# Kernel tuning notes

Measured on AMD Instinct MI355X. Metric: run time of the kernel, lower is better.

Reference implementation:

```python
import jax, jax.numpy as jnp
import numpy as np

NEG = -9e15
EPS = 1e-5

# GraphAttention (classic GAT layer): h = xW; e_ij = LeakyReLU(a1.h_i + a2.h_j);
# attention = softmax(where(adj>0, e, -9e15)); out = attention @ h.
# The torch code builds one big block-diagonal adjacency; off-block entries get
# -9e15 and underflow to exactly 0 after softmax, so batched per-block GAT is
# numerically identical and avoids the O((B*N)^2) dense waste.

def gat(x, adj, W, a1, a2):
    h = jnp.einsum('bnf,fh->bnh', x, W)
    e = jax.nn.leaky_relu(jnp.einsum('bnh,h->bn', h, a1)[:, :, None]
                          + jnp.einsum('bnh,h->bn', h, a2)[:, None, :], 0.2)
    att = jax.nn.softmax(jnp.where(adj > 0, e, NEG), axis=-1)
    return jnp.einsum('bnm,bmh->bnh', att, h)

def mlp(x, W1, b1, W2, b2):
    return jax.nn.relu(x @ W1 + b1) @ W2 + b2


def setup_inputs() -> dict:
    key = jax.random.key(0)
    ks = iter(jax.random.split(key, 40))
    B, NV, NO = 8, 500, 1500
    DV, DO, H = 512, 32, 128

    def mat(din, dout):
        return jax.random.normal(next(ks), (din, dout), jnp.float32) / np.sqrt(din)

    def vec(d):
        return jax.random.normal(next(ks), (d,), jnp.float32) * 0.1

    inp = {
        'vis_memory': jax.random.normal(next(ks), (B, NV, DV), jnp.float32),
        'obj_memory': jax.random.normal(next(ks), (B, NO, DO), jnp.float32),
        'vis_adj': jax.random.uniform(next(ks), (B, NV, NV), jnp.float32),
        'obj_adj': jax.random.uniform(next(ks), (B, NO, NO), jnp.float32),
        'object_A_OV': jax.random.uniform(next(ks), (B, NO, NV), jnp.float32),
        # GAT layers
        'Wv1': mat(DV, H), 'av1a': vec(H), 'av1b': vec(H),
        'Wv2': mat(H, H),  'av2a': vec(H), 'av2b': vec(H),
        'Wo1': mat(DO, H), 'ao1a': vec(H), 'ao1b': vec(H),
        'Wo2': mat(H, H),  'ao2a': vec(H), 'ao2b': vec(H),
        # globalTobject / objectTglobal MLPs
        'g2o_W1': mat(H, H), 'g2o_b1': jnp.zeros((H,), jnp.float32),
        'g2o_W2': mat(H, H), 'g2o_b2': jnp.zeros((H,), jnp.float32),
        'o2g_W1': mat(H, H), 'o2g_b1': jnp.zeros((H,), jnp.float32),
        'o2g_W2': mat(H, H), 'o2g_b2': jnp.zeros((H,), jnp.float32),
        # output projections
        'img_W': mat(H, DV), 'img_b': jnp.zeros((DV,), jnp.float32),
        'obj_W': mat(H, DO), 'obj_b': jnp.zeros((DO,), jnp.float32),
    }
    return inp


def reference(vis_memory, obj_memory, vis_adj, obj_adj, object_A_OV,
              Wv1, av1a, av1b, Wv2, av2a, av2b,
              Wo1, ao1a, ao1b, Wo2, ao2a, ao2b,
              g2o_W1, g2o_b1, g2o_W2, g2o_b2,
              o2g_W1, o2g_b1, o2g_W2, o2g_b2,
              img_W, img_b, obj_W, obj_b):
    # cross adjacencies (block-diagonal in torch -> batched here)
    vo = jnp.swapaxes(object_A_OV, 1, 2)            # (B, NV, NO)
    vo = vo / (vo.sum(2, keepdims=True) + EPS)
    ov = jnp.swapaxes(vo, 1, 2)                     # (B, NO, NV)
    ov = ov / (ov.sum(2, keepdims=True) + EPS)

    v1 = jax.nn.relu(gat(vis_memory, vis_adj, Wv1, av1a, av1b))
    o1 = jax.nn.relu(gat(obj_memory, obj_adj, Wo1, ao1a, ao1b))
    vis = v1 + mlp(jnp.einsum('bvo,boh->bvh', vo, o1), o2g_W1, o2g_b1, o2g_W2, o2g_b2)
    obj = o1 + mlp(jnp.einsum('bov,bvh->boh', ov, v1), g2o_W1, g2o_b1, g2o_W2, g2o_b2)

    v2 = jax.nn.relu(gat(vis, vis_adj, Wv2, av2a, av2b))
    o2 = jax.nn.relu(gat(obj, obj_adj, Wo2, ao2a, ao2b))
    vis = v2 + mlp(jnp.einsum('bvo,boh->bvh', vo, o2), o2g_W1, o2g_b1, o2g_W2, o2g_b2)
    obj = o2 + mlp(jnp.einsum('bov,bvh->boh', ov, v2), g2o_W1, g2o_b1, g2o_W2, g2o_b2)

    vis_out = vis @ img_W + img_b                   # (B, NV, DV)
    obj_out = obj @ obj_W + obj_b                   # (B, NO, DO)
    return (vis_out, obj_out)
```

## Files before the change

### kernel.cpp

```cpp
#include <hip/hip_runtime.h>
#include <math.h>

#define EPSV 1e-5f
#define HD 128
#define IT 64
#define JT 32
#define WP 68
#define CCH 16
#define THR 256

typedef __attribute__((address_space(3))) uint32_t lds_u32_t;
typedef __attribute__((address_space(1))) uint32_t gbl_u32_t;
typedef __attribute__((ext_vector_type(8))) short bf16x8;
typedef __attribute__((ext_vector_type(4))) float f32x4;

__device__ __forceinline__ void async_copy16(const float* g, float* l) {
    __builtin_amdgcn_global_load_lds((const gbl_u32_t*)g, (lds_u32_t*)l, 16, 0, 0);
}

__device__ __forceinline__ void stage_tile_async(const float* gsrc, float* lds, int t) {
    int wv = t >> 6, lane = t & 63;
#pragma unroll
    for (int it = 0; it < 4; ++it) {
        int c = it * 4 + wv;
        async_copy16(gsrc + c * 256 + lane * 4, lds + c * 256);
    }
}

__device__ __forceinline__ void stage_8k(const void* g, void* l, int t) {
    const float* gf = (const float*)g; float* lf = (float*)l;
    async_copy16(gf + t * 4, lf + t * 4);
    async_copy16(gf + t * 4 + 1024, lf + t * 4 + 1024);
}

__device__ __forceinline__ unsigned int f2bf(float f) {
    return __builtin_bit_cast(unsigned int, f) >> 16;
}

__device__ __forceinline__ unsigned short rne_bf16(float f) {
    unsigned int u = __builtin_bit_cast(unsigned int, f);
    u += 0x7FFFu + ((u >> 16) & 1u);
    return (unsigned short)(u >> 16);
}

struct WprepP { const float *W, *a1, *a2; unsigned short* WT; float *wa1, *wa2; int K; };
struct XprepP { const float* X; unsigned short* Xbf; const float *wa1, *wa2;
                float *sa, *sb; int rows; };
struct GmfP   { const unsigned short *Xbf, *WT; unsigned short* hT; int N, tilesJ; };
struct AggP  { const unsigned int* mask; const float *sa, *sb, *sm; const unsigned short* hT;
               float* out; int N, tiles, tilesJ; };
struct CrossP{ const float *A, *src, *rs1; float *pp; int iN, jN, tiles, tps; };
struct MlpP  { const float *pp, *scale; int S; const float *W1, *b1, *W2, *b2, *res;
               float *out; int rows; };


__global__ void colsum_part_k(const float* __restrict__ A, float* __restrict__ s1p,
                              int B, int NO, int NV) {
    int v = blockIdx.x * 256 + threadIdx.x;
    int c = blockIdx.y, b = blockIdx.z;
    if (v >= NV) return;
    int chunk = (NO + CCH - 1) / CCH;
    int o0 = c * chunk;
    int o1 = o0 + chunk; if (o1 > NO) o1 = NO;
    const float* Ab = A + (size_t)b * NO * NV + v;
    float s = 0.f;
    for (int o = o0; o < o1; ++o) s += Ab[(size_t)o * NV];
    s1p[((size_t)b * CCH + c) * NV + v] = s;
}

__global__ void colsum_fin_k(const float* __restrict__ s1p, float* __restrict__ rs1,
                             int B, int NV) {
    int idx = blockIdx.x * 256 + threadIdx.x;
    if (idx >= B * NV) return;
    int b = idx / NV, v = idx - b * NV;
    float s = 0.f;
    for (int c = 0; c < CCH; ++c) s += s1p[((size_t)b * CCH + c) * NV + v];
    rs1[idx] = 1.f / (s + EPSV);
}

__global__ void rowsum_inv_k(const float* __restrict__ A, const float* __restrict__ rs1,
                             float* __restrict__ rs2, int B, int NO, int NV) {
    int row = blockIdx.x * (blockDim.x >> 6) + (threadIdx.x >> 6);
    int lane = threadIdx.x & 63;
    if (row >= B * NO) return;
    int b = row / NO;
    const float* Ar = A + (size_t)row * NV;
    const float* r1 = rs1 + (size_t)b * NV;
    float s = 0.f;
    for (int v = lane; v < NV; v += 64) s += Ar[v] * r1[v];
    for (int off = 32; off; off >>= 1) s += __shfl_xor(s, off, 64);
    if (lane == 0) rs2[row] = 1.f / (s + EPSV);
}

template<int N, int TILESJ>
__global__ __launch_bounds__(256)
void maskg_k(const float* __restrict__ adj, unsigned int* __restrict__ maskT) {
    int tid = blockIdx.x * 256 + threadIdx.x;
    int w = tid % TILESJ;
    int rowid = tid / TILESJ;
    if (rowid >= 8 * N) return;
    int b = rowid / N, i = rowid - b * N;
    int j0 = w * 32;
    const float* src = adj + (size_t)rowid * N + j0;
    unsigned int bits = 0u;
    if (j0 + 32 <= N) {
#pragma unroll
        for (int q = 0; q < 8; ++q) {
            float4 v = ((const float4*)src)[q];
            bits |= (v.x > 0.f ? 1u : 0u) << (q * 4 + 0);
            bits |= (v.y > 0.f ? 1u : 0u) << (q * 4 + 1);
            bits |= (v.z > 0.f ? 1u : 0u) << (q * 4 + 2);
            bits |= (v.w > 0.f ? 1u : 0u) << (q * 4 + 3);
        }
    } else {
#pragma unroll
        for (int r = 0; r < 32; ++r)
            if (j0 + r < N) bits |= (src[r] > 0.f ? 1u : 0u) << r;
    }
    maskT[((size_t)b * TILESJ + w) * N + i] = bits;
}

__global__ __launch_bounds__(256)
void wprep_k(WprepP p0, WprepP p1, WprepP p2, WprepP p3, int e0, int e1, int e2) {
    __shared__ float lw[32][129];
    __shared__ float a1s[128], a2s[128];
    int bid = blockIdx.x;
    const WprepP& P = bid < e0 ? p0 : bid < e1 ? p1 : bid < e2 ? p2 : p3;
    int lb = bid < e0 ? bid : bid < e1 ? bid - e0 : bid < e2 ? bid - e1 : bid - e2;
    int k0 = lb * 32, K = P.K;
    int t = threadIdx.x;
    if (t < 128) { a1s[t] = P.a1[t]; a2s[t] = P.a2[t]; }
    for (int idx = t; idx < 32 * 32; idx += 256) {
        int kk = idx >> 5, c4 = idx & 31;
        float4 v = ((const float4*)(P.W + (size_t)(k0 + kk) * 128))[c4];
        lw[kk][c4 * 4 + 0] = v.x; lw[kk][c4 * 4 + 1] = v.y;
        lw[kk][c4 * 4 + 2] = v.z; lw[kk][c4 * 4 + 3] = v.w;
    }
    __syncthreads();
    int kk = t >> 3, g = t & 7;
    float s1 = 0.f, s2 = 0.f;
    for (int c = g; c < 128; c += 8) {
        float w = lw[kk][c];
        s1 = fmaf(w, a1s[c], s1);
        s2 = fmaf(w, a2s[c], s2);
    }
    s1 += __shfl_xor(s1, 1, 64); s1 += __shfl_xor(s1, 2, 64); s1 += __shfl_xor(s1, 4, 64);
    s2 += __shfl_xor(s2, 1, 64); s2 += __shfl_xor(s2, 2, 64); s2 += __shfl_xor(s2, 4, 64);
    if (g == 0) { P.wa1[k0 + kk] = s1; P.wa2[k0 + kk] = s2; }
    for (int idx = t; idx < 4096; idx += 256) {
        int c = idx >> 5, k = idx & 31;
        P.WT[(size_t)c * K + k0 + k] = rne_bf16(lw[k][c]);
    }
}

template<int K>
__device__ void xprep_body(const XprepP& P, int lb) {
    int t = threadIdx.x, wv = t >> 6, lane = t & 63;
    int row = lb * 4 + wv;
    if (row >= P.rows) return;
    const float4* x4 = (const float4*)(P.X + (size_t)row * K);
    const float4* w14 = (const float4*)P.wa1;
    const float4* w24 = (const float4*)P.wa2;
    unsigned short* xb = P.Xbf + (size_t)row * K;
    float s1 = 0.f, s2 = 0.f;
    constexpr int K4 = K / 4;
    constexpr int NI = (K4 + 63) / 64;
#pragma unroll
    for (int i = 0; i < NI; ++i) {
        int k4 = i * 64 + lane;
        if ((K4 % 64 == 0) || (k4 < K4)) {
            float4 x = x4[k4];
            float4 a = w14[k4];
            float4 b = w24[k4];
            s1 += x.x * a.x + x.y * a.y + x.z * a.z + x.w * a.w;
            s2 += x.x * b.x + x.y * b.y + x.z * b.z + x.w * b.w;
            ushort4 p = make_ushort4(rne_bf16(x.x), rne_bf16(x.y),
                                     rne_bf16(x.z), rne_bf16(x.w));
            *(ushort4*)(xb + (size_t)k4 * 4) = p;
        }
    }
#pragma unroll
    for (int off = 32; off; off >>= 1) {
        s1 += __shfl_xor(s1, off, 64);
        s2 += __shfl_xor(s2, off, 64);
    }
    if (lane == 0) { P.sa[row] = s1; P.sb[row] = s2; }
}

template<int KV, int KO>
__global__ __launch_bounds__(256)
void xprep2_k(XprepP V, XprepP O, int GV) {
    int bid = blockIdx.x;
    if (bid < GV) xprep_body<KV>(V, bid);
    else          xprep_body<KO>(O, bid - GV);
}

template<int K>
__device__ void gmf_body(const GmfP& P, int lb) {
    int tilesJ = P.tilesJ, N = P.N;
    int b = lb / tilesJ, jt = lb - b * tilesJ;
    int t = threadIdx.x, wv = t >> 6, lane = t & 63;
    int ml = lane & 15, quad = lane >> 4;
    const unsigned short* xb = P.Xbf + ((size_t)b * N + (size_t)jt * 32) * K;
    const unsigned short* wt0 = P.WT + (size_t)(wv * 32 + ml) * K;
    const unsigned short* wt1 = wt0 + (size_t)16 * K;
    const unsigned short* xb0 = xb + (size_t)ml * K;
    const unsigned short* xb1 = xb + (size_t)(16 + ml) * K;
    f32x4 acc00 = {0.f, 0.f, 0.f, 0.f}, acc01 = acc00, acc10 = acc00, acc11 = acc00;
#pragma unroll 4
    for (int kt = 0; kt < K / 32; ++kt) {
        int kk = kt * 32 + quad * 8;
        bf16x8 a0 = *(const bf16x8*)(wt0 + kk);
        bf16x8 a1 = *(const bf16x8*)(wt1 + kk);
        bf16x8 b0 = *(const bf16x8*)(xb0 + kk);
        bf16x8 b1 = *(const bf16x8*)(xb1 + kk);
        acc00 = __builtin_amdgcn_mfma_f32_16x16x32_bf16(a0, b0, acc00, 0, 0, 0);
        acc01 = __builtin_amdgcn_mfma_f32_16x16x32_bf16(a0, b1, acc01, 0, 0, 0);
        acc10 = __builtin_amdgcn_mfma_f32_16x16x32_bf16(a1, b0, acc10, 0, 0, 0);
        acc11 = __builtin_amdgcn_mfma_f32_16x16x32_bf16(a1, b1, acc11, 0, 0, 0);
    }
    unsigned short* hb = P.hT + (size_t)(b * tilesJ + jt) * 4096;
    int nvalid = N - jt * 32; if (nvalid > 32) nvalid = 32;
    bool ok0 = ml < nvalid, ok1 = (16 + ml) < nvalid;
    int c0 = wv * 32 + quad * 4;
#pragma unroll
    for (int r = 0; r < 4; ++r) {
        int ca = c0 + r, cb = c0 + 16 + r;
        int swa = ((ca >> 1) & 3) << 3, swb = ((cb >> 1) & 3) << 3;
        hb[ca * 32 + (ml ^ swa)]        = ok0 ? rne_bf16(acc00[r]) : 0;
        hb[ca * 32 + ((16 + ml) ^ swa)] = ok1 ? rne_bf16(acc01[r]) : 0;
        hb[cb * 32 + (ml ^ swb)]        = ok0 ? rne_bf16(acc10[r]) : 0;
        hb[cb * 32 + ((16 + ml) ^ swb)] = ok1 ? rne_bf16(acc11[r]) : 0;
    }
}

template<int KV, int KO>
__global__ __launch_bounds__(256)
void gmf2_k(GmfP V, GmfP O, int GV) {
    int bid = blockIdx.x;
    if (bid < GV) gmf_body<KV>(V, bid);
    else          gmf_body<KO>(O, bid - GV);
}

__global__ __launch_bounds__(256)
void sbmax2_k(const float* __restrict__ sbV, float* __restrict__ smV,
              const float* __restrict__ sbO, float* __restrict__ smO,
              int NV, int NO) {
    __shared__ float red[256];
    int b0 = blockIdx.x, t = threadIdx.x;
    const float* sb; float* out; int N;
    if (b0 < 8) { sb = sbV + (size_t)b0 * NV; out = smV + b0; N = NV; }
    else        { sb = sbO + (size_t)(b0 - 8) * NO; out = smO + (b0 - 8); N = NO; }
    float m = -INFINITY;
    for (int j = t; j < N; j += 256) m = fmaxf(m, sb[j]);
    red[t] = m; __syncthreads();
    for (int s = 128; s; s >>= 1) {
        if (t < s) red[t] = fmaxf(red[t], red[t + s]);
        __syncthreads();
    }
    if (t == 0) *out = red[0];
}

struct SharedAggM {
    unsigned short hsT[3][128][32];
    unsigned short wsA[2][4][64][8];
    unsigned int mask_s[48][64];
    float sb_s[48 * 32];
    float sa_s[IT], m_s[IT], z_s[IT];
};

__device__ void agg_body(SharedAggM& sm, const AggP& P, int lbid) {
    int tiles = P.tiles;
    int b = lbid / tiles;
    int i0 = (lbid - b * tiles) * IT;
    int N = P.N;
    int T = P.tilesJ;
    int t = threadIdx.x;
    if (t < IT) {
        int i = i0 + t;
        float s = (i < N) ? P.sa[(size_t)b * N + i] : 0.f;
        sm.sa_s[t] = s;
        float e = s + P.sm[b];
        sm.m_s[t] = e > 0.f ? e : 0.2f * e;
    }
    for (int idx = t; idx < (T << 6); idx += 256) {
        int w = idx >> 6, r = idx & 63;
        int ir = i0 + r;
        sm.mask_s[w][r] = (ir < N)
            ? P.mask[((size_t)b * T + w) * N + ir] : 0u;
    }
    const float* sbb = P.sb + (size_t)b * N;
    for (int idx = t; idx < (T << 5); idx += 256) {
        sm.sb_s[idx] = (idx < N) ? sbb[idx] : 0.f;
    }
    __syncthreads();
    const unsigned short* hTb = P.hT + (size_t)b * T * 4096;
    stage_8k(hTb, &sm.hsT[0][0][0], t);
    stage_8k(hTb + 4096, &sm.hsT[1][0][0], t);

    int wv = t >> 6, lane = t & 63;
    int il = t >> 2, j4 = (t & 3) * 4;
    int q0 = j4 >> 3, i0w = j4 & 7, wrow = il & 15;
    int nquad = lane >> 4, nlow = lane & 15;
    int nq2 = (nquad ^ ((nlow >> 1) & 3)) * 8;
    f32x4 acc[8];
#pragma unroll
    for (int nt = 0; nt < 8; ++nt)
#pragma unroll
        for (int r = 0; r < 4; ++r) acc[nt][r] = 0.f;
    float zacc = 0.f;
    const float4* sb4 = (const float4*)sm.sb_s;
    for (int tt = 0; tt < T; ++tt) {
        int cur = tt - (tt / 3) * 3;
        unsigned int mw = sm.mask_s[tt][il];
        float4 sA = sb4[tt * 8 + (t & 3)];
        float4 sB = sb4[tt * 8 + (t & 3) + 4];
        float sai = sm.sa_s[il], m = sm.m_s[il];
#pragma unroll
        for (int k = 0; k < 2; ++k) {
            float sv[4];
            { float4 s4 = k ? sB : sA; sv[0] = s4.x; sv[1] = s4.y; sv[2] = s4.z; sv[3] = s4.w; }
            float w_[4];
#pragma unroll
            for (int r = 0; r < 4; ++r) {
                float e = sai + sv[r];
                e = e > 0.f ? e : 0.2f * e;
                float ww = __expf(e - m);
                ww = ((mw >> (j4 + k * 16 + r)) & 1u) ? ww : 0.f;
                zacc += ww;
                w_[r] = ww;
            }
            unsigned int lo = f2bf(w_[0]) | (__builtin_bit_cast(unsigned int, w_[1]) & 0xFFFF0000u);
            unsigned int hi = f2bf(w_[2]) | (__builtin_bit_cast(unsigned int, w_[3]) & 0xFFFF0000u);
            *(uint2*)&sm.wsA[tt & 1][wv][wrow + 16 * (q0 + 2 * k)][i0w] = make_uint2(lo, hi);
        }
        if (tt + 1 < T) asm volatile("s_waitcnt vmcnt(2) lgkmcnt(0)" ::: "memory");
        else            asm volatile("s_waitcnt vmcnt(0) lgkmcnt(0)" ::: "memory");
        __builtin_amdgcn_s_barrier();
        asm volatile("" ::: "memory");
        if (tt + 2 < T) {
            int nb = tt + 2; nb -= (nb / 3) * 3;
            stage_8k(hTb + (size_t)(tt + 2) * 4096, &sm.hsT[nb][0][0], t);
        }
        bf16x8 afrag = *(const bf16x8*)&sm.wsA[tt & 1][wv][lane][0];
#pragma unroll
        for (int nt = 0; nt < 8; ++nt) {
            bf16x8 bfrag = *(const bf16x8*)&sm.hsT[cur][nt * 16 + nlow][nq2];
            acc[nt] = __builtin_amdgcn_mfma_f32_16x16x32_bf16(afrag, bfrag, acc[nt], 0, 0, 0);
        }
    }
    zacc += __shfl_xor(zacc, 1, 64);
    zacc += __shfl_xor(zacc, 2, 64);
    if ((t & 3) == 0) sm.z_s[il] = zacc;
    __syncthreads();
    float inv[4];
#pragma unroll
    for (int r = 0; r < 4; ++r) inv[r] = 1.f / sm.z_s[wv * 16 + nquad * 4 + r];
    float* outb = P.out + (size_t)b * N * HD;
#pragma unroll
    for (int nt = 0; nt < 8; ++nt)
#pragma unroll
        for (int r = 0; r < 4; ++r) {
            int row = i0 + wv * 16 + nquad * 4 + r;
            if (row < N)
                outb[(size_t)row * HD + nt * 16 + nlow] = fmaxf(acc[nt][r] * inv[r], 0.f);
        }
}

__global__ __launch_bounds__(256)
void agg2_k(AggP V, AggP O, int GVb) {
    __shared__ SharedAggM sm;
    int bid = blockIdx.x;
    if (bid < GVb) agg_body(sm, V, bid);
    else           agg_body(sm, O, bid - GVb);
}

__device__ __forceinline__ void tile_fma256(const float (*hs)[HD], const float (*ws)[WP],
                                            int rg, int c0, float acc[4][8]) {
#pragma unroll 8
    for (int jl = 0; jl < JT; ++jl) {
        float4 h0 = *(const float4*)&hs[jl][c0];
        float4 h1 = *(const float4*)&hs[jl][c0 + 64];
        float4 w4 = *(const float4*)&ws[jl][rg * 4];
        float wq[4] = {w4.x, w4.y, w4.z, w4.w};
#pragma unroll
        for (int q = 0; q < 4; ++q) {
            float w = wq[q];
            acc[q][0] = fmaf(w, h0.x, acc[q][0]);
            acc[q][1] = fmaf(w, h0.y, acc[q][1]);
            acc[q][2] = fmaf(w, h0.z, acc[q][2]);
            acc[q][3] = fmaf(w, h0.w, acc[q][3]);
            acc[q][4] = fmaf(w, h1.x, acc[q][4]);
            acc[q][5] = fmaf(w, h1.y, acc[q][5]);
            acc[q][6] = fmaf(w, h1.z, acc[q][6]);
            acc[q][7] = fmaf(w, h1.w, acc[q][7]);
        }
    }
}

__device__ __forceinline__ void part_store256(float* __restrict__ pp, size_t base,
                                              int i0, int N, int rg, int c0,
                                              float acc[4][8]) {
#pragma unroll
    for (int q = 0; q < 4; ++q) {
        int i = i0 + rg * 4 + q;
        if (i >= N) continue;
        float* op = pp + base + (size_t)i * HD;
        *(float4*)&op[c0]      = make_float4(acc[q][0], acc[q][1], acc[q][2], acc[q][3]);
        *(float4*)&op[c0 + 64] = make_float4(acc[q][4], acc[q][5], acc[q][6], acc[q][7]);
    }
}

struct SharedTile { float hs[2][JT][HD]; float ws[2][JT][WP]; };

__device__ void cross_vo_body(SharedTile& sm, const CrossP& P, int lbid) {
    int tiles = P.tiles;
    int split = lbid / (8 * tiles);
    int rem = lbid - split * 8 * tiles;
    int b = rem / tiles;
    int i0 = (rem - b * tiles) * IT;
    int NVl = P.iN, NOl = P.jN;
    int j_begin = split * P.tps * JT;
    if (j_begin >= NOl) return;
    int j_end = j_begin + P.tps * JT;
    if (j_end > NOl) j_end = NOl;
    int T = (j_end - j_begin + JT - 1) / JT;
    int t = threadIdx.x;
    int rg = t >> 4, c0 = (t & 15) * 4;
    int il = t & 63, jlb = t >> 6;
    float acc[4][8];
#pragma unroll
    for (int q = 0; q < 4; ++q)
#pragma unroll
        for (int x = 0; x < 8; ++x) acc[q][x] = 0.f;
    const float* Ab = P.A + (size_t)b * NOl * NVl;
    const float* srcb = P.src + (size_t)b * NOl * HD;
    int v = i0 + il;
    float w8[8];
    stage_tile_async(srcb + (size_t)j_begin * HD, &sm.hs[0][0][0], t);
#pragma unroll
    for (int k = 0; k < 8; ++k) {
        int o = j_begin + jlb + k * 4;
        w8[k] = (v < NVl && o < NOl) ? Ab[(size_t)o * NVl + v] : 0.f;
    }
    for (int tt = 0; tt < T; ++tt) {
        int cur = tt & 1;
#pragma unroll
        for (int k = 0; k < 8; ++k) sm.ws[cur][jlb + k * 4][il] = w8[k];
        __syncthreads();
        if (tt + 1 < T) {
            int jn = j_begin + (tt + 1) * JT;
            stage_tile_async(srcb + (size_t)jn * HD, &sm.hs[1 - cur][0][0], t);
#pragma unroll
            for (int k = 0; k < 8; ++k) {
                int o = jn + jlb + k * 4;
                w8[k] = (v < NVl && o < NOl) ? Ab[(size_t)o * NVl + v] : 0.f;
            }
        }
        tile_fma256(sm.hs[cur], sm.ws[cur], rg, c0, acc);
    }
    size_t rowsTot = (size_t)8 * NVl;
    part_store256(P.pp, ((size_t)split * rowsTot + (size_t)b * NVl) * HD, i0, NVl, rg, c0, acc);
}

__device__ void cross_ov_body(SharedTile& sm, const CrossP& P, int lbid) {
    int tiles = P.tiles;
    int split = lbid / (8 * tiles);
    int rem = lbid - split * 8 * tiles;
    int b = rem / tiles;
    int i0 = (rem - b * tiles) * IT;
    int NOl = P.iN, NVl = P.jN;
    int j_begin = split * P.tps * JT;
    if (j_begin >= NVl) return;
    int j_end = j_begin + P.tps * JT;
    if (j_end > NVl) j_end = NVl;
    int T = (j_end - j_begin + JT - 1) / JT;
    int t = threadIdx.x;
    int rg = t >> 4, c0 = (t & 15) * 4;
    int il = t >> 2, j4 = (t & 3) * 4;
    float acc[4][8];
#pragma unroll
    for (int q = 0; q < 4; ++q)
#pragma unroll
        for (int x = 0; x < 8; ++x) acc[q][x] = 0.f;
    const float* Ab = P.A + (size_t)b * NOl * NVl;
    const float* srcb = P.src + (size_t)b * NVl * HD;
    const float* r1b = P.rs1 + (size_t)b * NVl;
    int orow = i0 + il;
    float4 a4[2], r4[2];
    stage_tile_async(srcb + (size_t)j_begin * HD, &sm.hs[0][0][0], t);
#pragma unroll
    for (int k = 0; k < 2; ++k) {
        int vv = j_begin + j4 + k * 16;
        float4 av = make_float4(0.f,0.f,0.f,0.f), rv = make_float4(0.f,0.f,0.f,0.f);
        if (orow < NOl) {
            if (vv + 3 < NVl) {
                av = *(const float4*)&Ab[(size_t)orow * NVl + vv];
                rv = *(const float4*)&r1b[vv];
            } else {
                float* ap = (float*)&av; float* rp = (float*)&rv;
                for (int r = 0; r < 4; ++r)
                    if (vv + r < NVl) { ap[r] = Ab[(size_t)orow * NVl + vv + r]; rp[r] = r1b[vv + r]; }
            }
        }
        a4[k] = av; r4[k] = rv;
    }
    for (int tt = 0; tt < T; ++tt) {
        int cur = tt & 1;
#pragma unroll
        for (int k = 0; k < 2; ++k) {
            float wv[4] = {a4[k].x * r4[k].x, a4[k].y * r4[k].y,
                           a4[k].z * r4[k].z, a4[k].w * r4[k].w};
#pragma unroll
            for (int r = 0; r < 4; ++r) sm.ws[cur][j4 + r + k * 16][il] = wv[r];
        }
        __syncthreads();
        if (tt + 1 < T) {
            int jn = j_begin + (tt + 1) * JT;
            stage_tile_async(srcb + (size_t)jn * HD, &sm.hs[1 - cur][0][0], t);
#pragma unroll
            for (int k = 0; k < 2; ++k) {
                int vv = jn + j4 + k * 16;
                float4 av = make_float4(0.f,0.f,0.f,0.f), rv = make_float4(0.f,0.f,0.f,0.f);
                if (orow < NOl) {
                    if (vv + 3 < NVl) {
                        av = *(const float4*)&Ab[(size_t)orow * NVl + vv];
                        rv = *(const float4*)&r1b[vv];
                    } else {
                        float* ap = (float*)&av; float* rp = (float*)&rv;
                        for (int r = 0; r < 4; ++r)
                            if (vv + r < NVl) { ap[r] = Ab[(size_t)orow * NVl + vv + r]; rp[r] = r1b[vv + r]; }
                    }
                }
                a4[k] = av; r4[k] = rv;
            }
        }
        tile_fma256(sm.hs[cur], sm.ws[cur], rg, c0, acc);
    }
    size_t rowsTot = (size_t)8 * NOl;
    part_store256(P.pp, ((size_t)split * rowsTot + (size_t)b * NOl) * HD, i0, NOl, rg, c0, acc);
}

__global__ __launch_bounds__(256)
void cross2_k(CrossP VO, CrossP OV, int GVOb) {
    __shared__ SharedTile sm;
    int bid = blockIdx.x;
    if (bid < GVOb) cross_vo_body(sm, VO, bid);
    else            cross_ov_body(sm, OV, bid - GVOb);
}

__global__ __launch_bounds__(128)
void mlp2_k(MlpP V, MlpP O, int GVb) {
    __shared__ float xs[8][HD];
    __shared__ float hh[8][HD];
    int bid = blockIdx.x;
    const MlpP& P = (bid < GVb) ? V : O;
    int row0 = ((bid < GVb) ? bid : bid - GVb) * 8;
    int rows = P.rows;
    int t = threadIdx.x;
    for (int l = t; l < 8 * 32; l += 128) {
        int r = l >> 5, c4 = l & 31;
        int row = row0 + r;
        float4 v = make_float4(0.f, 0.f, 0.f, 0.f);
        if (row < rows) {
            for (int s = 0; s < P.S; ++s) {
                float4 p = ((const float4*)P.pp)[((size_t)s * rows + row) * 32 + c4];
                v.x += p.x; v.y += p.y; v.z += p.z; v.w += p.w;
            }
            float sc = P.scale[row];
            v.x *= sc; v.y *= sc; v.z *= sc; v.w *= sc;
        }
        ((float4*)&xs[r][0])[c4] = v;
    }
    __syncthreads();
    int wv = t >> 6, tt = t & 63, rb = wv * 4;
    float a0[4] = {0.f, 0.f, 0.f, 0.f}, a1v[4] = {0.f, 0.f, 0.f, 0.f};
#pragma unroll 4
    for (int k = 0; k < HD; ++k) {
        float w0 = P.W1[(size_t)k * HD + tt];
        float w1 = P.W1[(size_t)k * HD + tt + 64];
#pragma unroll
        for (int r = 0; r < 4; ++r) {
            float x = xs[rb + r][k];
            a0[r] = fmaf(x, w0, a0[r]);
            a1v[r] = fmaf(x, w1, a1v[r]);
        }
    }
    float bb0 = P.b1[tt], bb1 = P.b1[tt + 64];
#pragma unroll
    for (int r = 0; r < 4; ++r) {
        hh[rb + r][tt]      = fmaxf(a0[r] + bb0, 0.f);
        hh[rb + r][tt + 64] = fmaxf(a1v[r] + bb1, 0.f);
    }
    __syncthreads();
    float c0a[4] = {0.f, 0.f, 0.f, 0.f}, c1a[4] = {0.f, 0.f, 0.f, 0.f};
#pragma unroll 4
    for (int k = 0; k < HD; ++k) {
        float w0 = P.W2[(size_t)k * HD + tt];
        float w1 = P.W2[(size_t)k * HD + tt + 64];
#pragma unroll
        for (int r = 0; r < 4; ++r) {
            float x = hh[rb + r][k];
            c0a[r] = fmaf(x, w0, c0a[r]);
            c1a[r] = fmaf(x, w1, c1a[r]);
        }
    }
    float d0 = P.b2[tt], d1 = P.b2[tt + 64];
#pragma unroll
    for (int r = 0; r < 4; ++r) {
        int row = row0 + rb + r;
        if (row >= rows) continue;
        P.out[(size_t)row * HD + tt]      = c0a[r] + d0 + P.res[(size_t)row * HD + tt];
        P.out[(size_t)row * HD + tt + 64] = c1a[r] + d1 + P.res[(size_t)row * HD + tt + 64];
    }
}

template<int RELU, int BIAS, int RES>
__global__ __launch_bounds__(128)
void linear_k(const float* __restrict__ X, const float* __restrict__ W,
              const float* __restrict__ bias, const float* __restrict__ res,
              float* __restrict__ out, int rows, int K, int Dout) {
    __shared__ float xs[4][512];
    int row0 = blockIdx.x * 4;
    int t = threadIdx.x;
    int K4 = K >> 2;
    for (int l = t; l < 4 * K4; l += 128) {
        int r = l / K4, c4 = l - r * K4;
        float4 val = make_float4(0.f, 0.f, 0.f, 0.f);
        if (row0 + r < rows) val = ((const float4*)(X + (size_t)(row0 + r) * K))[c4];
        ((float4*)&xs[r][0])[c4] = val;
    }
    __syncthreads();
    int chunk = Dout < 256 ? Dout : 256;
    int half = chunk >> 1;
    if (t >= half) return;
    int c0 = blockIdx.y * chunk + t;
    int c1 = c0 + half;
    float a00 = 0, a01 = 0, a02 = 0, a03 = 0, a10 = 0, a11 = 0, a12 = 0, a13 = 0;
#pragma unroll 4
    for (int k = 0; k < K; ++k) {
        float w0 = W[(size_t)k * Dout + c0];
        float w1 = W[(size_t)k * Dout + c1];
        float x0 = xs[0][k], x1 = xs[1][k], x2 = xs[2][k], x3 = xs[3][k];
        a00 = fmaf(x0, w0, a00); a01 = fmaf(x1, w0, a01);
        a02 = fmaf(x2, w0, a02); a03 = fmaf(x3, w0, a03);
        a10 = fmaf(x0, w1, a10); a11 = fmaf(x1, w1, a11);
        a12 = fmaf(x2, w1, a12); a13 = fmaf(x3, w1, a13);
    }
    float accs[2][4] = {{a00, a01, a02, a03}, {a10, a11, a12, a13}};
    int cs[2] = {c0, c1};
    for (int h = 0; h < 2; ++h) {
        float bv = BIAS ? bias[cs[h]] : 0.f;
        for (int r = 0; r < 4; ++r) {
            int row = row0 + r;
            if (row >= rows) continue;
            float v = accs[h][r] + bv;
            if (RES) v += res[(size_t)row * Dout + cs[h]];
            if (RELU) v = fmaxf(v, 0.f);
            out[(size_t)row * Dout + cs[h]] = v;
        }
    }
}

extern "C" void kernel_launch(void* const* d_in, const int* in_sizes, int n_in,
                              void* d_out, int out_size, void* d_ws, size_t ws_size,
                              hipStream_t stream) {
    const int B = 8, NV = 500, NO = 1500, DV = 512, DO = 32;
    const float* vis_memory = (const float*)d_in[0];
    const float* obj_memory = (const float*)d_in[1];
    const float* vis_adj    = (const float*)d_in[2];
    const float* obj_adj    = (const float*)d_in[3];
    const float* A_OV       = (const float*)d_in[4];
    const float* Wv1  = (const float*)d_in[5];
    const float* av1a = (const float*)d_in[6];
    const float* av1b = (const float*)d_in[7];
    const float* Wv2  = (const float*)d_in[8];
    const float* av2a = (const float*)d_in[9];
    const float* av2b = (const float*)d_in[10];
    const float* Wo1  = (const float*)d_in[11];
    const float* ao1a = (const float*)d_in[12];
    const float* ao1b = (const float*)d_in[13];
    const float* Wo2  = (const float*)d_in[14];
    const float* ao2a = (const float*)d_in[15];
    const float* ao2b = (const float*)d_in[16];
    const float* g2o_W1 = (const float*)d_in[17];
    const float* g2o_b1 = (const float*)d_in[18];
    const float* g2o_W2 = (const float*)d_in[19];
    const float* g2o_b2 = (const float*)d_in[20];
    const float* o2g_W1 = (const float*)d_in[21];
    const float* o2g_b1 = (const float*)d_in[22];
    const float* o2g_W2 = (const float*)d_in[23];
    const float* o2g_b2 = (const float*)d_in[24];
    const float* img_W = (const float*)d_in[25];
    const float* img_b = (const float*)d_in[26];
    const float* obj_W = (const float*)d_in[27];
    const float* obj_b = (const float*)d_in[28];

    const int tilesJV = 16, tilesJO = 47;

    float* wsp = (float*)d_ws;
    size_t off = 0;
    auto alloc = [&](size_t n) { float* p = wsp + off; off += (n + 3) & ~(size_t)3; return p; };
    float* rs1   = alloc(B * NV);
    float* rs2   = alloc(B * NO);
    float* saV   = alloc(B * NV);
    float* sbV   = alloc(B * NV);
    float* smV   = alloc(B);
    float* saO   = alloc(B * NO);
    float* sbO   = alloc(B * NO);
    float* smO   = alloc(B);
    float* s1p   = alloc((size_t)B * CCH * NV);
    unsigned int* maskV = (unsigned int*)alloc((size_t)B * tilesJV * NV);
    unsigned int* maskO = (unsigned int*)alloc((size_t)B * tilesJO * NO);
    unsigned short* WTv1 = (unsigned short*)alloc(128 * 512 / 2);
    unsigned short* WTo1 = (unsigned short*)alloc(128 * 32 / 2);
    unsigned short* WTv2 = (unsigned short*)alloc(128 * 128 / 2);
    unsigned short* WTo2 = (unsigned short*)alloc(128 * 128 / 2);
    float* wav1a = alloc(512); float* wav1b = alloc(512);
    float* wao1a = alloc(32);  float* wao1b = alloc(32);
    float* wav2a = alloc(128); float* wav2b = alloc(128);
    float* wao2a = alloc(128); float* wao2b = alloc(128);
    unsigned short* XbfV = (unsigned short*)alloc((size_t)B * NV * 512 / 2);
    unsigned short* XbfO = (unsigned short*)alloc((size_t)B * NO * 128 / 2);
    unsigned short* hTv = (unsigned short*)alloc((size_t)B * tilesJV * 4096 / 2);
    unsigned short* hTo = (unsigned short*)alloc((size_t)B * tilesJO * 4096 / 2);
    float* v1    = alloc((size_t)B * NV * HD);
    float* o1    = alloc((size_t)B * NO * HD);
    float* visb  = alloc((size_t)B * NV * HD);
    float* objb  = alloc((size_t)B * NO * HD);
    float* ppV   = alloc((size_t)8 * B * NV * HD);
    float* ppO   = alloc((size_t)4 * B * NO * HD);
    alloc(16384);

    {
        WprepP w0{Wv1, av1a, av1b, WTv1, wav1a, wav1b, DV};
        WprepP w1{Wo1, ao1a, ao1b, WTo1, wao1a, wao1b, DO};
        WprepP w2{Wv2, av2a, av2b, WTv2, wav2a, wav2b, HD};
        WprepP w3{Wo2, ao2a, ao2b, WTo2, wao2a, wao2b, HD};
        wprep_k<<<25, 256, 0, stream>>>(w0, w1, w2, w3, 16, 17, 21);
    }
    maskg_k<500, 16><<<(8 * 500 * 16 + 255) / 256, 256, 0, stream>>>(vis_adj, maskV);
    maskg_k<1500, 47><<<(8 * 1500 * 47 + 255) / 256, 256, 0, stream>>>(obj_adj, maskO);

    colsum_part_k<<<dim3((NV + 255) / 256, CCH, B), 256, 0, stream>>>(A_OV, s1p, B, NO, NV);
    colsum_fin_k<<<dim3((B * NV + 255) / 256), 256, 0, stream>>>(s1p, rs1, B, NV);
    rowsum_inv_k<<<dim3((B * NO + 3) / 4), 256, 0, stream>>>(A_OV, rs1, rs2, B, NO, NV);

    const int tilesV = 8, tilesO = 24;
    const int SVO = 8, SOV = 4;
    const int tpsVO = 6;
    const int tpsOV = 4;
    const int G_AGG_V = B * tilesV;
    const int G_AGG_O = B * tilesO;
    const int G_CR_VO = B * tilesV * SVO;
    const int G_CR_OV = B * tilesO * SOV;
    const int G_MLP_V = B * NV / 8;
    const int G_MLP_O = B * NO / 8;
    const int G_XP_V = B * NV / 4;
    const int G_XP_O = B * NO / 4;
    const int G_GMF_V = B * tilesJV;
    const int G_GMF_O = B * tilesJO;

    auto tail = [&](float* visout, float* objout) {
        sbmax2_k<<<16, 256, 0, stream>>>(sbV, smV, sbO, smO, NV, NO);
        AggP av{maskV, saV, sbV, smV, hTv, v1, NV, tilesV, tilesJV};
        AggP ao{maskO, saO, sbO, smO, hTo, o1, NO, tilesO, tilesJO};
        agg2_k<<<G_AGG_V + G_AGG_O, THR, 0, stream>>>(av, ao, G_AGG_V);
        CrossP cvo{A_OV, o1, nullptr, ppV, NV, NO, tilesV, tpsVO};
        CrossP cov{A_OV, v1, rs1, ppO, NO, NV, tilesO, tpsOV};
        cross2_k<<<G_CR_VO + G_CR_OV, THR, 0, stream>>>(cvo, cov, G_CR_VO);
        MlpP mv{ppV, rs1, SVO, o2g_W1, o2g_b1, o2g_W2, o2g_b2, v1, visout, B * NV};
        MlpP mo{ppO, rs2, SOV, g2o_W1, g2o_b1, g2o_W2, g2o_b2, o1, objout, B * NO};
        mlp2_k<<<G_MLP_V + G_MLP_O, 128, 0, stream>>>(mv, mo, G_MLP_V);
    };

    {
        XprepP xv{vis_memory, XbfV, wav1a, wav1b, saV, sbV, B * NV};
        XprepP xo{obj_memory, XbfO, wao1a, wao1b, saO, sbO, B * NO};
        xprep2_k<512, 32><<<G_XP_V + G_XP_O, 256, 0, stream>>>(xv, xo, G_XP_V);
        GmfP gv{XbfV, WTv1, hTv, NV, tilesJV};
        GmfP go{XbfO, WTo1, hTo, NO, tilesJO};
        gmf2_k<512, 32><<<G_GMF_V + G_GMF_O, 256, 0, stream>>>(gv, go, G_GMF_V);
        tail(visb, objb);
    }
    {
        XprepP xv{visb, XbfV, wav2a, wav2b, saV, sbV, B * NV};
        XprepP xo{objb, XbfO, wao2a, wao2b, saO, sbO, B * NO};
        xprep2_k<128, 128><<<G_XP_V + G_XP_O, 256, 0, stream>>>(xv, xo, G_XP_V);
        GmfP gv{XbfV, WTv2, hTv, NV, tilesJV};
        GmfP go{XbfO, WTo2, hTo, NO, tilesJO};
        gmf2_k<128, 128><<<G_GMF_V + G_GMF_O, 256, 0, stream>>>(gv, go, G_GMF_V);
        tail(visb, objb);
    }

    float* vis_out = (float*)d_out;
    float* obj_out = vis_out + (size_t)B * NV * DV;
    linear_k<0, 1, 0><<<dim3((B * NV + 3) / 4, (DV + 255) / 256), 128, 0, stream>>>(
        visb, img_W, img_b, nullptr, vis_out, B * NV, HD, DV);
    linear_k<0, 1, 0><<<dim3((B * NO + 3) / 4, 1), 128, 0, stream>>>(
        objb, obj_W, obj_b, nullptr, obj_out, B * NO, HD, DO);
}
```

Measured before the change: 634.4 us.

## Restructure GAT aggregation into 32-row tiles with register-built MFMA A fragments

The attention-aggregation kernel now handles 32 query rows per block with 128 threads instead of 64 rows with 256 threads, roughly doubling the number of blocks. Each lane computes its own 8 softmax weights and packs them straight into the bf16 MFMA A operand, dropping the shared-memory staging buffer for the weights. The async prefetch of hT tiles deepens from a 3-buffer to a 5-buffer ring with matching waitcnt values. In exchange, mask and sb loads now run past N without bounds checks, relying on padding and mask bits to zero out the extra rows and columns.

```diff
diff --git a/kernel.cpp b/kernel.cpp
--- a/kernel.cpp
+++ b/kernel.cpp
@@ -27,10 +27,12 @@
     }
 }
 
-__device__ __forceinline__ void stage_8k(const void* g, void* l, int t) {
+__device__ __forceinline__ void stage_8k_128(const void* g, void* l, int t) {
     const float* gf = (const float*)g; float* lf = (float*)l;
     async_copy16(gf + t * 4, lf + t * 4);
+    async_copy16(gf + t * 4 + 512, lf + t * 4 + 512);
     async_copy16(gf + t * 4 + 1024, lf + t * 4 + 1024);
+    async_copy16(gf + t * 4 + 1536, lf + t * 4 + 1536);
 }
 
 __device__ __forceinline__ unsigned int f2bf(float f) {
@@ -261,115 +263,107 @@
     if (t == 0) *out = red[0];
 }
 
-struct SharedAggM {
-    unsigned short hsT[3][128][32];
-    unsigned short wsA[2][4][64][8];
-    unsigned int mask_s[48][64];
+struct SharedAgg32 {
+    unsigned short hsT[5][128][32];
+    unsigned int mask_s[48][32];
     float sb_s[48 * 32];
-    float sa_s[IT], m_s[IT], z_s[IT];
+    float z_s[32];
 };
 
-__device__ void agg_body(SharedAggM& sm, const AggP& P, int lbid) {
+__device__ void agg_body(SharedAgg32& sm, const AggP& P, int lbid) {
     int tiles = P.tiles;
     int b = lbid / tiles;
-    int i0 = (lbid - b * tiles) * IT;
-    int N = P.N;
-    int T = P.tilesJ;
+    int i0 = (lbid - b * tiles) * 32;
+    int N = P.N, T = P.tilesJ;
     int t = threadIdx.x;
-    if (t < IT) {
-        int i = i0 + t;
-        float s = (i < N) ? P.sa[(size_t)b * N + i] : 0.f;
-        sm.sa_s[t] = s;
-        float e = s + P.sm[b];
-        sm.m_s[t] = e > 0.f ? e : 0.2f * e;
-    }
-    for (int idx = t; idx < (T << 6); idx += 256) {
-        int w = idx >> 6, r = idx & 63;
-        int ir = i0 + r;
-        sm.mask_s[w][r] = (ir < N)
-            ? P.mask[((size_t)b * T + w) * N + ir] : 0u;
+    int wv = t >> 6, lane = t & 63, quad = lane >> 4, ml = lane & 15;
+    const unsigned int* mb = P.mask + (size_t)b * T * N + i0;
+    for (int idx = t; idx < T * 8; idx += 128) {
+        int w = idx >> 3, r4 = idx & 7;
+        *(uint4*)&sm.mask_s[w][r4 * 4] = *(const uint4*)&mb[(size_t)w * N + r4 * 4];
     }
     const float* sbb = P.sb + (size_t)b * N;
-    for (int idx = t; idx < (T << 5); idx += 256) {
-        sm.sb_s[idx] = (idx < N) ? sbb[idx] : 0.f;
-    }
+    for (int idx = t; idx < T * 8; idx += 128)
+        ((float4*)sm.sb_s)[idx] = ((const float4*)sbb)[idx];
+    int row_loc = wv * 16 + ml;
+    int irow = i0 + row_loc;
+    float sa = (irow < N) ? P.sa[(size_t)b * N + irow] : 0.f;
+    float e0 = sa + P.sm[b];
+    float m = e0 > 0.f ? e0 : 0.2f * e0;
     __syncthreads();
     const unsigned short* hTb = P.hT + (size_t)b * T * 4096;
-    stage_8k(hTb, &sm.hsT[0][0][0], t);
-    stage_8k(hTb + 4096, &sm.hsT[1][0][0], t);
-
-    int wv = t >> 6, lane = t & 63;
-    int il = t >> 2, j4 = (t & 3) * 4;
-    int q0 = j4 >> 3, i0w = j4 & 7, wrow = il & 15;
-    int nquad = lane >> 4, nlow = lane & 15;
-    int nq2 = (nquad ^ ((nlow >> 1) & 3)) * 8;
+    stage_8k_128(hTb, &sm.hsT[0][0][0], t);
+    if (T > 1) stage_8k_128(hTb + 4096, &sm.hsT[1][0][0], t);
+    if (T > 2) stage_8k_128(hTb + 8192, &sm.hsT[2][0][0], t);
+    if (T > 3) stage_8k_128(hTb + 12288, &sm.hsT[3][0][0], t);
+
+    int nq2 = (quad ^ ((ml >> 1) & 3)) * 8;
     f32x4 acc[8];
 #pragma unroll
     for (int nt = 0; nt < 8; ++nt)
 #pragma unroll
         for (int r = 0; r < 4; ++r) acc[nt][r] = 0.f;
     float zacc = 0.f;
-    const float4* sb4 = (const float4*)sm.sb_s;
     for (int tt = 0; tt < T; ++tt) {
-        int cur = tt - (tt / 3) * 3;
-        unsigned int mw = sm.mask_s[tt][il];
-        float4 sA = sb4[tt * 8 + (t & 3)];
-        float4 sB = sb4[tt * 8 + (t & 3) + 4];
-        float sai = sm.sa_s[il], m = sm.m_s[il];
-#pragma unroll
-        for (int k = 0; k < 2; ++k) {
-            float sv[4];
-            { float4 s4 = k ? sB : sA; sv[0] = s4.x; sv[1] = s4.y; sv[2] = s4.z; sv[3] = s4.w; }
-            float w_[4];
-#pragma unroll
-            for (int r = 0; r < 4; ++r) {
-                float e = sai + sv[r];
-                e = e > 0.f ? e : 0.2f * e;
-                float ww = __expf(e - m);
-                ww = ((mw >> (j4 + k * 16 + r)) & 1u) ? ww : 0.f;
-                zacc += ww;
-                w_[r] = ww;
-            }
-            unsigned int lo = f2bf(w_[0]) | (__builtin_bit_cast(unsigned int, w_[1]) & 0xFFFF0000u);
-            unsigned int hi = f2bf(w_[2]) | (__builtin_bit_cast(unsigned int, w_[3]) & 0xFFFF0000u);
-            *(uint2*)&sm.wsA[tt & 1][wv][wrow + 16 * (q0 + 2 * k)][i0w] = make_uint2(lo, hi);
-        }
-        if (tt + 1 < T) asm volatile("s_waitcnt vmcnt(2) lgkmcnt(0)" ::: "memory");
-        else            asm volatile("s_waitcnt vmcnt(0) lgkmcnt(0)" ::: "memory");
+        int cur = tt - (tt / 5) * 5;
+        unsigned int mq = sm.mask_s[tt][row_loc] >> (quad * 8);
+        float4 s0 = *(const float4*)&sm.sb_s[tt * 32 + quad * 8];
+        float4 s1 = *(const float4*)&sm.sb_s[tt * 32 + quad * 8 + 4];
+        float sv[8] = {s0.x, s0.y, s0.z, s0.w, s1.x, s1.y, s1.z, s1.w};
+        float w_[8];
+#pragma unroll
+        for (int i = 0; i < 8; ++i) {
+            float e = sa + sv[i];
+            e = e > 0.f ? e : 0.2f * e;
+            float ww = __expf(e - m);
+            ww = ((mq >> i) & 1u) ? ww : 0.f;
+            zacc += ww;
+            w_[i] = ww;
+        }
+        unsigned int u0 = f2bf(w_[0]) | (__builtin_bit_cast(unsigned int, w_[1]) & 0xFFFF0000u);
+        unsigned int u1 = f2bf(w_[2]) | (__builtin_bit_cast(unsigned int, w_[3]) & 0xFFFF0000u);
+        unsigned int u2 = f2bf(w_[4]) | (__builtin_bit_cast(unsigned int, w_[5]) & 0xFFFF0000u);
+        unsigned int u3 = f2bf(w_[6]) | (__builtin_bit_cast(unsigned int, w_[7]) & 0xFFFF0000u);
+        uint4 af = make_uint4(u0, u1, u2, u3);
+        bf16x8 afrag = __builtin_bit_cast(bf16x8, af);
+        int rem = T - tt;
+        if (rem >= 4)      asm volatile("s_waitcnt vmcnt(12)" ::: "memory");
+        else if (rem == 3) asm volatile("s_waitcnt vmcnt(8)" ::: "memory");
+        else if (rem == 2) asm volatile("s_waitcnt vmcnt(4)" ::: "memory");
+        else               asm volatile("s_waitcnt vmcnt(0)" ::: "memory");
         __builtin_amdgcn_s_barrier();
         asm volatile("" ::: "memory");
-        if (tt + 2 < T) {
-            int nb = tt + 2; nb -= (nb / 3) * 3;
-            stage_8k(hTb + (size_t)(tt + 2) * 4096, &sm.hsT[nb][0][0], t);
-        }
-        bf16x8 afrag = *(const bf16x8*)&sm.wsA[tt & 1][wv][lane][0];
+        if (tt + 4 < T) {
+            int nb = tt + 4; nb -= (nb / 5) * 5;
+            stage_8k_128(hTb + (size_t)(tt + 4) * 4096, &sm.hsT[nb][0][0], t);
+        }
 #pragma unroll
         for (int nt = 0; nt < 8; ++nt) {
-            bf16x8 bfrag = *(const bf16x8*)&sm.hsT[cur][nt * 16 + nlow][nq2];
+            bf16x8 bfrag = *(const bf16x8*)&sm.hsT[cur][nt * 16 + ml][nq2];
             acc[nt] = __builtin_amdgcn_mfma_f32_16x16x32_bf16(afrag, bfrag, acc[nt], 0, 0, 0);
         }
     }
-    zacc += __shfl_xor(zacc, 1, 64);
-    zacc += __shfl_xor(zacc, 2, 64);
-    if ((t & 3) == 0) sm.z_s[il] = zacc;
+    zacc += __shfl_xor(zacc, 16, 64);
+    zacc += __shfl_xor(zacc, 32, 64);
+    if (quad == 0) sm.z_s[row_loc] = zacc;
     __syncthreads();
-    float inv[4];
-#pragma unroll
-    for (int r = 0; r < 4; ++r) inv[r] = 1.f / sm.z_s[wv * 16 + nquad * 4 + r];
     float* outb = P.out + (size_t)b * N * HD;
 #pragma unroll
-    for (int nt = 0; nt < 8; ++nt)
-#pragma unroll
-        for (int r = 0; r < 4; ++r) {
-            int row = i0 + wv * 16 + nquad * 4 + r;
-            if (row < N)
-                outb[(size_t)row * HD + nt * 16 + nlow] = fmaxf(acc[nt][r] * inv[r], 0.f);
-        }
-}
-
-__global__ __launch_bounds__(256)
+    for (int r = 0; r < 4; ++r) {
+        int rr = wv * 16 + quad * 4 + r;
+        float inv = 1.f / sm.z_s[rr];
+        int row = i0 + rr;
+        if (row < N) {
+#pragma unroll
+            for (int nt = 0; nt < 8; ++nt)
+                outb[(size_t)row * HD + nt * 16 + ml] = fmaxf(acc[nt][r] * inv, 0.f);
+        }
+    }
+}
+
+__global__ __launch_bounds__(128)
 void agg2_k(AggP V, AggP O, int GVb) {
-    __shared__ SharedAggM sm;
+    __shared__ SharedAgg32 sm;
     int bid = blockIdx.x;
     if (bid < GVb) agg_body(sm, V, bid);
     else           agg_body(sm, O, bid - GVb);
@@ -746,12 +740,13 @@
     colsum_fin_k<<<dim3((B * NV + 255) / 256), 256, 0, stream>>>(s1p, rs1, B, NV);
     rowsum_inv_k<<<dim3((B * NO + 3) / 4), 256, 0, stream>>>(A_OV, rs1, rs2, B, NO, NV);
 
+    const int tilesV32 = 16, tilesO32 = 47;
     const int tilesV = 8, tilesO = 24;
     const int SVO = 8, SOV = 4;
     const int tpsVO = 6;
     const int tpsOV = 4;
-    const int G_AGG_V = B * tilesV;
-    const int G_AGG_O = B * tilesO;
+    const int G_AGG_V = B * tilesV32;
+    const int G_AGG_O = B * tilesO32;
     const int G_CR_VO = B * tilesV * SVO;
     const int G_CR_OV = B * tilesO * SOV;
     const int G_MLP_V = B * NV / 8;
@@ -763,9 +758,9 @@
 
     auto tail = [&](float* visout, float* objout) {
         sbmax2_k<<<16, 256, 0, stream>>>(sbV, smV, sbO, smO, NV, NO);
-        AggP av{maskV, saV, sbV, smV, hTv, v1, NV, tilesV, tilesJV};
-        AggP ao{maskO, saO, sbO, smO, hTo, o1, NO, tilesO, tilesJO};
-        agg2_k<<<G_AGG_V + G_AGG_O, THR, 0, stream>>>(av, ao, G_AGG_V);
+        AggP av{maskV, saV, sbV, smV, hTv, v1, NV, tilesV32, tilesJV};
+        AggP ao{maskO, saO, sbO, smO, hTo, o1, NO, tilesO32, tilesJO};
+        agg2_k<<<G_AGG_V + G_AGG_O, 128, 0, stream>>>(av, ao, G_AGG_V);
         CrossP cvo{A_OV, o1, nullptr, ppV, NV, NO, tilesV, tpsVO};
         CrossP cov{A_OV, v1, rs1, ppO, NO, NV, tilesO, tpsOV};
         cross2_k<<<G_CR_VO + G_CR_OV, THR, 0, stream>>>(cvo, cov, G_CR_VO);
```

New measurement: 589.0 us. 7.1% less time.
